# Performance work log

Hardware: AMD Instinct MI355X
Metric: run time of the kernel (lower is better)

## Reference

```python
import jax, jax.numpy as jnp
import numpy as np

B, C_ATT, C_VAL = 1, 64, 64
T, H, W = 40, 32, 32
HW = H * W
TOPK = 10
TEMP = 0.07
NEIGHBOR_RANGE = 24  # circle mode -> radius = 24 // 2
NON_MASK_LEN = 1     # first frame is not masked
NEG_INF = -1e30


def _spatial_neighbor_circle(h, w, neighbor_range):
    """Circle-mode spatial neighbor mask, (h*w, h*w) bool."""
    radius = neighbor_range // 2
    gy, gx = jnp.meshgrid(jnp.arange(h, dtype=jnp.float32),
                          jnp.arange(w, dtype=jnp.float32), indexing='ij')
    dy = gy[:, :, None, None] - gy[None, None, :, :]
    dx = gx[:, :, None, None] - gx[None, None, :, :]
    dist = jnp.sqrt(dy * dy + dx * dx)
    return (dist < radius).reshape(h * w, h * w)


def setup_inputs() -> dict:
    key0 = jax.random.key(0)
    k1, k2, k3 = jax.random.split(key0, 3)
    query = jax.random.normal(k1, (B, C_ATT, H, W), dtype=jnp.float32)
    key = jax.random.normal(k2, (B, C_ATT, T, H, W), dtype=jnp.float32)
    value = jax.random.normal(k3, (B, C_VAL, T, H, W), dtype=jnp.float32)
    mask = _spatial_neighbor_circle(H, W, NEIGHBOR_RANGE)  # (HW, HW) bool
    return {"query": query, "key": key, "value": value, "mask": mask}


def _l2_normalize(x, axis, eps=1e-12):
    # matches F.normalize(p=2): x / max(||x||, eps)
    n = jnp.sqrt(jnp.sum(x * x, axis=axis, keepdims=True))
    return x / jnp.maximum(n, eps)


def reference(query, key, value, mask):
    # normalize along channel dim
    q = _l2_normalize(query, axis=1).reshape(B, C_ATT, HW)          # (B,C,Q)
    k = _l2_normalize(key, axis=1).reshape(B, C_ATT, T * HW)        # (B,C,K)
    v = value.reshape(B, C_VAL, T * HW)                             # (B,Cv,K)

    # affinity over all keys vs all queries (chunking in the original is a
    # pure memory optimization; the math per query column is identical)
    aff = jnp.einsum('bck,bcq->bkq', k, q) / TEMP                   # (B,K,Q)

    # build full mask: first NON_MASK_LEN frames fully visible, remaining
    # frames restricted to the spatial-neighbor circle
    tiled = jnp.tile(mask, (T - NON_MASK_LEN, 1))                   # ((T-nm)*HW, Q)
    full_mask = jnp.concatenate(
        [jnp.ones((NON_MASK_LEN * HW, HW), dtype=bool), tiled], axis=0)  # (K,Q)
    aff = jnp.where(full_mask[None], aff, NEG_INF)

    # top-k over the key dimension, per query
    aff_qk = jnp.swapaxes(aff, 1, 2)                                # (B,Q,K)
    top_vals, top_idx = jax.lax.top_k(aff_qk, TOPK)                 # (B,Q,topk)
    weights = jax.nn.softmax(top_vals, axis=-1)                     # (B,Q,topk)

    # gather top-k values: (B,Cv,Q,topk)
    gathered = jnp.take_along_axis(v[:, :, None, :], top_idx[:, None, :, :], axis=3)
    out = jnp.einsum('bcqk,bqk->bcq', gathered, weights)            # (B,Cv,Q)
    return out.reshape(B, C_VAL, H, W)
```

## Files before the change

### kernel.cpp

```cpp
#include <hip/hip_runtime.h>
#include <hip/hip_bf16.h>
#include <float.h>

#define HWQ   1024
#define NK    40960
#define NCH   64
#define NTOP  10
#define NF0JOB 8
#define PVLEN (NF0JOB * NTOP)
#define CAPG  384
#define R2    144
#define TOTU  23556
#define NBLK  4096
#define TSCALE 14.2857142857142857f
#define LOSCL  4.8828125e-4f

typedef _Float16 f16x8 __attribute__((ext_vector_type(8)));
typedef float    f32x4 __attribute__((ext_vector_type(4)));
typedef unsigned short us8 __attribute__((ext_vector_type(8)));
typedef unsigned long long u64;
typedef unsigned int       u32;

__device__ inline float bf16bits_to_f32(unsigned short u) {
    union { u32 i; float f; } z; z.i = ((u32)u) << 16; return z.f;
}
__device__ inline unsigned short f32_to_bf16bits(float x) {
    __hip_bfloat16 b = __float2bfloat16(x);
    return *(unsigned short*)&b;
}

__device__ inline int sniff_fp32(const unsigned short* __restrict__ raw) {
    const int lane = threadIdx.x & 63;
    const int e = (raw[lane] >> 7) & 0xFF;
    const u64 m = __ballot(e < 100 || e > 133);
    return __popcll(m) > 16;
}

__device__ inline u32 ord32(float v) {
    const u32 b = __float_as_uint(v);
    return b ^ (u32)(((int)b >> 31) | (int)0x80000000);
}
__device__ inline u64 pack_vi(float val, int kidx) {
    return ((u64)ord32(val) << 16) | (u32)(0xFFFF - kidx);
}
__device__ inline float unpack_val(u64 p) {
    const u32 u = (u32)(p >> 16);
    const u32 b = u ^ (~((u32)((int)u >> 31)) | 0x80000000u);
    return __uint_as_float(b);
}
__device__ inline int unpack_idx(u64 p) { return 0xFFFF - (int)(p & 0xFFFF); }

__device__ inline void ins10(u64* v, u64 pk) {
#pragma unroll
    for (int j = NTOP - 1; j >= 1; --j) {
        const bool gj = pk > v[j];
        const bool gp = pk > v[j - 1];
        v[j] = gj ? (gp ? v[j - 1] : pk) : v[j];
    }
    if (pk > v[0]) v[0] = pk;
}

__global__ __launch_bounds__(256) void prep_all(
    const void* __restrict__ qin_, const void* __restrict__ kin_,
    const void* __restrict__ vin_,
    f16x8* __restrict__ kh, f16x8* __restrict__ kl,
    f16x8* __restrict__ qh, f16x8* __restrict__ ql,
    unsigned short* __restrict__ vt, int* __restrict__ cnt)
{
    __shared__ float ssq[4][64];
    const int isf  = sniff_fp32((const unsigned short*)kin_);
    const int bid  = blockIdx.x;
    const int tid  = threadIdx.x;
    const int w    = tid >> 6;
    const int lane = tid & 63;
    const int c0   = w * 16;

    if (bid == 655) {
        cnt[tid * 4 + 0] = 0; cnt[tid * 4 + 1] = 0;
        cnt[tid * 4 + 2] = 0; cnt[tid * 4 + 3] = 0;
    }

    if (bid < 640) {
        const int key = bid * 64 + lane;
        float x[16];
        if (isf) {
            const float* p = (const float*)kin_;
#pragma unroll
            for (int i = 0; i < 16; ++i) x[i] = p[(c0 + i) * NK + key];
        } else {
            const __hip_bfloat16* p = (const __hip_bfloat16*)kin_;
#pragma unroll
            for (int i = 0; i < 16; ++i) x[i] = __bfloat162float(p[(c0 + i) * NK + key]);
        }
        float s = 0.f;
#pragma unroll
        for (int i = 0; i < 16; ++i) s = fmaf(x[i], x[i], s);
        ssq[w][lane] = s;
        __syncthreads();
        s = ssq[0][lane] + ssq[1][lane] + ssq[2][lane] + ssq[3][lane];
        const float rn = 1.0f / fmaxf(sqrtf(s), 1e-12f);

        const int tb = (key >> 4) * 128 + (key & 15);
#pragma unroll
        for (int b2 = 0; b2 < 2; ++b2) {
            f16x8 h, l;
#pragma unroll
            for (int jj = 0; jj < 8; ++jj) {
                const float xv = x[b2 * 8 + jj] * rn;
                const _Float16 hh = (_Float16)xv;
                h[jj] = hh;
                l[jj] = (_Float16)((xv - (float)hh) * 2048.0f);
            }
            kh[tb + (w * 2 + b2) * 16] = h;
            kl[tb + (w * 2 + b2) * 16] = l;
        }

        unsigned short vv[16];
        if (isf) {
            const float* p = (const float*)vin_;
#pragma unroll
            for (int i = 0; i < 16; ++i) vv[i] = f32_to_bf16bits(p[(c0 + i) * NK + key]);
        } else {
            const unsigned short* p = (const unsigned short*)vin_;
#pragma unroll
            for (int i = 0; i < 16; ++i) vv[i] = p[(c0 + i) * NK + key];
        }
        us8* dst = (us8*)(vt + (size_t)key * NCH + c0);
#pragma unroll
        for (int b2 = 0; b2 < 2; ++b2) {
            us8 o;
#pragma unroll
            for (int e = 0; e < 8; ++e) o[e] = vv[b2 * 8 + e];
            dst[b2] = o;
        }
    } else {
        const int q = (bid - 640) * 64 + lane;
        float x[16];
        if (isf) {
            const float* p = (const float*)qin_;
#pragma unroll
            for (int i = 0; i < 16; ++i) x[i] = p[(c0 + i) * HWQ + q];
        } else {
            const __hip_bfloat16* p = (const __hip_bfloat16*)qin_;
#pragma unroll
            for (int i = 0; i < 16; ++i) x[i] = __bfloat162float(p[(c0 + i) * HWQ + q]);
        }
        float s = 0.f;
#pragma unroll
        for (int i = 0; i < 16; ++i) s = fmaf(x[i], x[i], s);
        ssq[w][lane] = s;
        __syncthreads();
        s = ssq[0][lane] + ssq[1][lane] + ssq[2][lane] + ssq[3][lane];
        const float rn = 1.0f / fmaxf(sqrtf(s), 1e-12f);

        const int tb = (q >> 4) * 128 + (q & 15);
#pragma unroll
        for (int b2 = 0; b2 < 2; ++b2) {
            f16x8 h, l;
#pragma unroll
            for (int jj = 0; jj < 8; ++jj) {
                const float xv = x[b2 * 8 + jj] * rn;
                const _Float16 hh = (_Float16)xv;
                h[jj] = hh;
                l[jj] = (_Float16)((xv - (float)hh) * 2048.0f);
            }
            qh[tb + (w * 2 + b2) * 16] = h;
            ql[tb + (w * 2 + b2) * 16] = l;
        }
    }
}

__device__ inline void quad_merge_store(
    u64 (*sm)[16][NTOP], int lane, u64* out10)
{
    int p0 = 0, p1 = 0, p2 = 0, p3 = 0;
#pragma unroll
    for (int r = 0; r < NTOP; ++r) {
        const u64 h0 = sm[0][lane][p0], h1 = sm[1][lane][p1];
        const u64 h2 = sm[2][lane][p2], h3 = sm[3][lane][p3];
        u64 m = h0; int sel = 0;
        if (h1 > m) { m = h1; sel = 1; }
        if (h2 > m) { m = h2; sel = 2; }
        if (h3 > m) { m = h3; sel = 3; }
        out10[r] = m;
        p0 += (sel == 0); p1 += (sel == 1); p2 += (sel == 2); p3 += (sel == 3);
    }
}

__global__ __launch_bounds__(128) void attn_f0(
    const f16x8* __restrict__ kh, const f16x8* __restrict__ kl,
    const f16x8* __restrict__ qh, const f16x8* __restrict__ ql,
    u64* __restrict__ pv)
{
    __shared__ u64 sm[2][4][16][NTOP];

    const int tid  = threadIdx.x;
    const int w    = tid >> 6;
    const int lane = tid & 63;
    const int quad = lane >> 4;
    const int n    = lane & 15;

    const int t   = blockIdx.x * 2 + w;
    const int job = blockIdx.y;

    const int qb = t * 128 + n;
    const f16x8 bh0 = qh[qb + quad * 16];
    const f16x8 bh1 = qh[qb + (4 + quad) * 16];
    const f16x8 bl0 = ql[qb + quad * 16];
    const f16x8 bl1 = ql[qb + (4 + quad) * 16];

    u64 v[NTOP];
#pragma unroll
    for (int jj = 0; jj < NTOP; ++jj) v[jj] = 0ull;

    const int start = job * 8, end = start + 8;
    const int loff = (n + quad * 16) * 16;
    const char* ph = (const char*)kh + (size_t)start * 2048 + loff;
    const char* pl = (const char*)kl + (size_t)start * 2048 + loff;

    for (int kt = start; kt < end; ++kt) {
        const f16x8 Ah0 = *(const f16x8*)(ph);
        const f16x8 Ah1 = *(const f16x8*)(ph + 1024);
        const f16x8 Al0 = *(const f16x8*)(pl);
        const f16x8 Al1 = *(const f16x8*)(pl + 1024);

        f32x4 accH = {0.f,0.f,0.f,0.f}, accL0 = {0.f,0.f,0.f,0.f}, accL1 = {0.f,0.f,0.f,0.f};
        accH  = __builtin_amdgcn_mfma_f32_16x16x32_f16(Ah0, bh0, accH, 0, 0, 0);
        accH  = __builtin_amdgcn_mfma_f32_16x16x32_f16(Ah1, bh1, accH, 0, 0, 0);
        accL0 = __builtin_amdgcn_mfma_f32_16x16x32_f16(Ah0, bl0, accL0, 0, 0, 0);
        accL0 = __builtin_amdgcn_mfma_f32_16x16x32_f16(Al0, bh0, accL0, 0, 0, 0);
        accL1 = __builtin_amdgcn_mfma_f32_16x16x32_f16(Ah1, bl1, accL1, 0, 0, 0);
        accL1 = __builtin_amdgcn_mfma_f32_16x16x32_f16(Al1, bh1, accL1, 0, 0, 0);

        const int key0 = kt * 16 + quad * 4;
#pragma unroll
        for (int r = 0; r < 4; ++r) {
            const float val = fmaf(accL0[r] + accL1[r], LOSCL, accH[r]);
            const u64 pk = pack_vi(val, key0 + r);
            if (pk > v[NTOP - 1]) ins10(v, pk);
        }
        ph += 2048; pl += 2048;
    }

#pragma unroll
    for (int jj = 0; jj < NTOP; ++jj) sm[w][quad][n][jj] = v[jj];
    __syncthreads();

    if (lane < 16) {
        u64 out10[NTOP];
        quad_merge_store(sm[w], lane, out10);
        const int q = t * 16 + lane;
#pragma unroll
        for (int r = 0; r < NTOP; ++r) pv[(size_t)q * PVLEN + job * NTOP + r] = out10[r];
    }
}

__global__ __launch_bounds__(256) void theta_refine(
    const u64* __restrict__ pv, float* __restrict__ thmax)
{
    const int q    = blockIdx.x * 4 + (threadIdx.x >> 6);
    const int lane = threadIdx.x & 63;

    u64 l0 = pv[(size_t)q * PVLEN + lane];
    u64 l1 = (lane < 16) ? pv[(size_t)q * PVLEN + 64 + lane] : 0ull;

    u64 m = 0ull;
#pragma unroll
    for (int r = 0; r < NTOP; ++r) {
        u64 c = l0 > l1 ? l0 : l1;
#pragma unroll
        for (int off = 32; off >= 1; off >>= 1) {
            const u32 lo = (u32)c, hi = (u32)(c >> 32);
            const u32 lo2 = (u32)__shfl_xor((int)lo, off);
            const u32 hi2 = (u32)__shfl_xor((int)hi, off);
            const u64 o = ((u64)hi2 << 32) | lo2;
            if (o > c) c = o;
        }
        if (l0 == c) l0 = 0ull;
        if (l1 == c) l1 = 0ull;
        m = c;
    }
    if (lane == 0) thmax[q] = unpack_val(m);
}

__global__ __launch_bounds__(64) void attn_masked(
    const f16x8* __restrict__ kh, const f16x8* __restrict__ kl,
    const f16x8* __restrict__ qh, const f16x8* __restrict__ ql,
    const float* __restrict__ thmax,
    u64* __restrict__ gcand, int* __restrict__ cnt)
{
    const int lane = threadIdx.x;
    const int quad = lane >> 4;
    const int n    = lane & 15;

    const int wid = (blockIdx.x & 7) * (NBLK / 8) + (blockIdx.x >> 3);
    const int u0  = (int)(((long long)wid * TOTU) >> 12);
    const int u1  = (int)(((long long)(wid + 1) * TOTU) >> 12);

    f16x8 b0h0, b0h1, b0l0, b0l1, b1h0, b1h1, b1l0, b1l1;
    float theta0 = 0.f, theta1 = 0.f;
    int cur_qy = -1, q0 = 0;

    for (int u = u0; u < u1; ++u) {
        const int fm1 = u / 604;
        const int rem = u - fm1 * 604;
        int qy, off;
        if (rem < 210) {
            int t = (int)((sqrtf((float)(529 + 8 * rem)) - 23.0f) * 0.5f);
            while ((t * (t + 23)) / 2 > rem) --t;
            while (((t + 1) * (t + 24)) / 2 <= rem) ++t;
            qy = t; off = rem - (t * (t + 23)) / 2;
        } else if (rem < 417) {
            qy = 12 + (rem - 210) / 23; off = (rem - 210) % 23;
        } else {
            const int s = 603 - rem;
            int t = (int)((sqrtf((float)(529 + 8 * s)) - 23.0f) * 0.5f);
            while ((t * (t + 23)) / 2 > s) --t;
            while (((t + 1) * (t + 24)) / 2 <= s) ++t;
            qy = 31 - t;
            off = (12 + t) - 1 - (s - (t * (t + 23)) / 2);
        }
        const int rlo = (qy > 11) ? qy - 11 : 0;
        const int row = rlo + off;
        const int frame = fm1 + 1;

        if (qy != cur_qy) {
            cur_qy = qy;
            const int qb = qy * 256 + n;
            b0h0 = qh[qb + quad * 16];       b0h1 = qh[qb + (4 + quad) * 16];
            b0l0 = ql[qb + quad * 16];       b0l1 = ql[qb + (4 + quad) * 16];
            b1h0 = qh[qb + 128 + quad * 16]; b1h1 = qh[qb + 128 + (4 + quad) * 16];
            b1l0 = ql[qb + 128 + quad * 16]; b1l1 = ql[qb + 128 + (4 + quad) * 16];
            q0 = qy * 32 + n;
            theta0 = thmax[q0];
            theta1 = thmax[q0 + 16];
        }

        const int dy   = row - qy;
        const int rem2 = R2 - dy * dy;
        const int tbase = frame * 64 + row * 2;
        const int keyrow = frame * 1024 + row * 32;

#pragma unroll 1
        for (int kt2 = 0; kt2 < 2; ++kt2) {
            const f16x8* pA = kh + (tbase + kt2) * 128 + n;
            const f16x8* pL = kl + (tbase + kt2) * 128 + n;
            const f16x8 ah0 = pA[quad * 16];
            const f16x8 ah1 = pA[(4 + quad) * 16];
            const f16x8 al0 = pL[quad * 16];
            const f16x8 al1 = pL[(4 + quad) * 16];

            f32x4 H0 = {0.f,0.f,0.f,0.f}, L00 = {0.f,0.f,0.f,0.f}, L01 = {0.f,0.f,0.f,0.f};
            f32x4 H1 = {0.f,0.f,0.f,0.f}, L10 = {0.f,0.f,0.f,0.f}, L11 = {0.f,0.f,0.f,0.f};
            H0  = __builtin_amdgcn_mfma_f32_16x16x32_f16(ah0, b0h0, H0, 0, 0, 0);
            H0  = __builtin_amdgcn_mfma_f32_16x16x32_f16(ah1, b0h1, H0, 0, 0, 0);
            L00 = __builtin_amdgcn_mfma_f32_16x16x32_f16(ah0, b0l0, L00, 0, 0, 0);
            L00 = __builtin_amdgcn_mfma_f32_16x16x32_f16(al0, b0h0, L00, 0, 0, 0);
            L01 = __builtin_amdgcn_mfma_f32_16x16x32_f16(ah1, b0l1, L01, 0, 0, 0);
            L01 = __builtin_amdgcn_mfma_f32_16x16x32_f16(al1, b0h1, L01, 0, 0, 0);
            H1  = __builtin_amdgcn_mfma_f32_16x16x32_f16(ah0, b1h0, H1, 0, 0, 0);
            H1  = __builtin_amdgcn_mfma_f32_16x16x32_f16(ah1, b1h1, H1, 0, 0, 0);
            L10 = __builtin_amdgcn_mfma_f32_16x16x32_f16(ah0, b1l0, L10, 0, 0, 0);
            L10 = __builtin_amdgcn_mfma_f32_16x16x32_f16(al0, b1h0, L10, 0, 0, 0);
            L11 = __builtin_amdgcn_mfma_f32_16x16x32_f16(ah1, b1l1, L11, 0, 0, 0);
            L11 = __builtin_amdgcn_mfma_f32_16x16x32_f16(al1, b1h1, L11, 0, 0, 0);

            const int kx0  = kt2 * 16 + quad * 4;
            const int key0 = keyrow + kx0;
#pragma unroll
            for (int r = 0; r < 4; ++r) {
                const float v0 = fmaf(L00[r] + L01[r], LOSCL, H0[r]);
                const float v1 = fmaf(L10[r] + L11[r], LOSCL, H1[r]);
                if (v0 > theta0) {
                    const int dx = kx0 + r - n;
                    if (dx * dx < rem2) {
                        const int pos = atomicAdd(&cnt[q0], 1);
                        if (pos < CAPG) gcand[(size_t)q0 * CAPG + pos] = pack_vi(v0, key0 + r);
                    }
                }
                if (v1 > theta1) {
                    const int dx = kx0 + r - 16 - n;
                    if (dx * dx < rem2) {
                        const int pos = atomicAdd(&cnt[q0 + 16], 1);
                        if (pos < CAPG) gcand[(size_t)(q0 + 16) * CAPG + pos] = pack_vi(v1, key0 + r);
                    }
                }
            }
        }
    }
}

__global__ __launch_bounds__(64) void finalize_kernel(
    const u64* __restrict__ pv, const u64* __restrict__ gcand,
    const int* __restrict__ cnt, const unsigned short* __restrict__ vt,
    const unsigned short* __restrict__ kin_raw, void* __restrict__ out_)
{
    const int isf  = sniff_fp32(kin_raw);
    const int q    = blockIdx.x;
    const int lane = threadIdx.x;

    u64 lv[8];
    lv[0] = pv[(size_t)q * PVLEN + lane];
    lv[1] = (lane < 16) ? pv[(size_t)q * PVLEN + 64 + lane] : 0ull;
    const int c = min(cnt[q], CAPG);
#pragma unroll
    for (int e = 0; e < 6; ++e) {
        const int idx = e * 64 + lane;
        lv[2 + e] = (idx < c) ? gcand[(size_t)q * CAPG + idx] : 0ull;
    }

    float wv[NTOP]; int wi[NTOP];
#pragma unroll
    for (int r = 0; r < NTOP; ++r) {
        u64 m = lv[0];
#pragma unroll
        for (int e = 1; e < 8; ++e) if (lv[e] > m) m = lv[e];
#pragma unroll
        for (int off = 32; off >= 1; off >>= 1) {
            const u32 lo = (u32)m, hi = (u32)(m >> 32);
            const u32 lo2 = (u32)__shfl_xor((int)lo, off);
            const u32 hi2 = (u32)__shfl_xor((int)hi, off);
            const u64 o = ((u64)hi2 << 32) | lo2;
            if (o > m) m = o;
        }
#pragma unroll
        for (int e = 0; e < 8; ++e) if (lv[e] == m) lv[e] = 0ull;
        wv[r] = unpack_val(m); wi[r] = unpack_idx(m);
    }

    float ww[NTOP]; float wsum = 0.f;
#pragma unroll
    for (int r = 0; r < NTOP; ++r) { ww[r] = expf((wv[r] - wv[0]) * TSCALE); wsum += ww[r]; }
    const float inv = 1.0f / wsum;

    float acc = 0.f;
#pragma unroll
    for (int r = 0; r < NTOP; ++r)
        acc += ww[r] * bf16bits_to_f32(vt[(size_t)wi[r] * NCH + lane]);
    const float res = acc * inv;

    if (isf) ((float*)out_)[lane * HWQ + q] = res;
    else     ((__hip_bfloat16*)out_)[lane * HWQ + q] = __float2bfloat16(res);
}

extern "C" void kernel_launch(void* const* d_in, const int* in_sizes, int n_in,
                              void* d_out, int out_size, void* d_ws, size_t ws_size,
                              hipStream_t stream)
{
    const void* qin = d_in[0];
    const void* kin = d_in[1];
    const void* vin = d_in[2];

    char* w = (char*)d_ws;
    f16x8*          kh    = (f16x8*)(w);
    f16x8*          kl    = (f16x8*)(w + 5242880);
    f16x8*          qhv   = (f16x8*)(w + 10485760);
    f16x8*          qlv   = (f16x8*)(w + 10616832);
    unsigned short* vt    = (unsigned short*)(w + 10747904);
    u64*            pv    = (u64*)(w + 15990784);
    u64*            gcand = (u64*)(w + 16646144);
    float*          thmax = (float*)(w + 19791872);
    int*            cnt   = (int*)(w + 19795968);

    prep_all<<<656, 256, 0, stream>>>(qin, kin, vin, kh, kl, qhv, qlv, vt, cnt);
    attn_f0<<<dim3(32, 8), 128, 0, stream>>>(kh, kl, qhv, qlv, pv);
    theta_refine<<<256, 256, 0, stream>>>(pv, thmax);
    attn_masked<<<NBLK, 64, 0, stream>>>(kh, kl, qhv, qlv, thmax, gcand, cnt);
    finalize_kernel<<<HWQ, 64, 0, stream>>>(pv, gcand, cnt, vt,
                                            (const unsigned short*)kin, d_out);
}
```

Measured before the change: 146.7 us.

## Fuse all stages into one cooperative persistent kernel with grid syncs

Replaces the five separate launches (prep, frame-0 attention, theta refine, masked attention, finalize) with a single cooperative kernel of 512 blocks. The stages are separated by grid-wide syncs. Frame-0 top-k is now done by 64 blocks with a four-wave merge, and the masked-candidate buffers are sharded per query (8 shards, padded counters) to reduce atomic contention. This is meant to remove launch gaps and inter-kernel overhead, at the cost of grid.sync latency, idle blocks during the frame-0 stage, and a smaller per-shard candidate capacity.

Measured after the change: 343.2 us. +134.0%, slower.

```diff
diff --git a/kernel.cpp b/kernel.cpp
--- a/kernel.cpp
+++ b/kernel.cpp
@@ -1,17 +1,18 @@
 #include <hip/hip_runtime.h>
+#include <hip/hip_cooperative_groups.h>
 #include <hip/hip_bf16.h>
 #include <float.h>
+
+namespace cg = cooperative_groups;
 
 #define HWQ   1024
 #define NK    40960
 #define NCH   64
 #define NTOP  10
-#define NF0JOB 8
-#define PVLEN (NF0JOB * NTOP)
-#define CAPG  384
+#define CAPS  64
 #define R2    144
 #define TOTU  23556
-#define NBLK  4096
+#define NWAVE 2048
 #define TSCALE 14.2857142857142857f
 #define LOSCL  4.8828125e-4f
 
@@ -60,124 +61,12 @@
     if (pk > v[0]) v[0] = pk;
 }
 
-__global__ __launch_bounds__(256) void prep_all(
-    const void* __restrict__ qin_, const void* __restrict__ kin_,
-    const void* __restrict__ vin_,
-    f16x8* __restrict__ kh, f16x8* __restrict__ kl,
-    f16x8* __restrict__ qh, f16x8* __restrict__ ql,
-    unsigned short* __restrict__ vt, int* __restrict__ cnt)
-{
-    __shared__ float ssq[4][64];
-    const int isf  = sniff_fp32((const unsigned short*)kin_);
-    const int bid  = blockIdx.x;
-    const int tid  = threadIdx.x;
-    const int w    = tid >> 6;
-    const int lane = tid & 63;
-    const int c0   = w * 16;
-
-    if (bid == 655) {
-        cnt[tid * 4 + 0] = 0; cnt[tid * 4 + 1] = 0;
-        cnt[tid * 4 + 2] = 0; cnt[tid * 4 + 3] = 0;
-    }
-
-    if (bid < 640) {
-        const int key = bid * 64 + lane;
-        float x[16];
-        if (isf) {
-            const float* p = (const float*)kin_;
-#pragma unroll
-            for (int i = 0; i < 16; ++i) x[i] = p[(c0 + i) * NK + key];
-        } else {
-            const __hip_bfloat16* p = (const __hip_bfloat16*)kin_;
-#pragma unroll
-            for (int i = 0; i < 16; ++i) x[i] = __bfloat162float(p[(c0 + i) * NK + key]);
-        }
-        float s = 0.f;
-#pragma unroll
-        for (int i = 0; i < 16; ++i) s = fmaf(x[i], x[i], s);
-        ssq[w][lane] = s;
-        __syncthreads();
-        s = ssq[0][lane] + ssq[1][lane] + ssq[2][lane] + ssq[3][lane];
-        const float rn = 1.0f / fmaxf(sqrtf(s), 1e-12f);
-
-        const int tb = (key >> 4) * 128 + (key & 15);
-#pragma unroll
-        for (int b2 = 0; b2 < 2; ++b2) {
-            f16x8 h, l;
-#pragma unroll
-            for (int jj = 0; jj < 8; ++jj) {
-                const float xv = x[b2 * 8 + jj] * rn;
-                const _Float16 hh = (_Float16)xv;
-                h[jj] = hh;
-                l[jj] = (_Float16)((xv - (float)hh) * 2048.0f);
-            }
-            kh[tb + (w * 2 + b2) * 16] = h;
-            kl[tb + (w * 2 + b2) * 16] = l;
-        }
-
-        unsigned short vv[16];
-        if (isf) {
-            const float* p = (const float*)vin_;
-#pragma unroll
-            for (int i = 0; i < 16; ++i) vv[i] = f32_to_bf16bits(p[(c0 + i) * NK + key]);
-        } else {
-            const unsigned short* p = (const unsigned short*)vin_;
-#pragma unroll
-            for (int i = 0; i < 16; ++i) vv[i] = p[(c0 + i) * NK + key];
-        }
-        us8* dst = (us8*)(vt + (size_t)key * NCH + c0);
-#pragma unroll
-        for (int b2 = 0; b2 < 2; ++b2) {
-            us8 o;
-#pragma unroll
-            for (int e = 0; e < 8; ++e) o[e] = vv[b2 * 8 + e];
-            dst[b2] = o;
-        }
-    } else {
-        const int q = (bid - 640) * 64 + lane;
-        float x[16];
-        if (isf) {
-            const float* p = (const float*)qin_;
-#pragma unroll
-            for (int i = 0; i < 16; ++i) x[i] = p[(c0 + i) * HWQ + q];
-        } else {
-            const __hip_bfloat16* p = (const __hip_bfloat16*)qin_;
-#pragma unroll
-            for (int i = 0; i < 16; ++i) x[i] = __bfloat162float(p[(c0 + i) * HWQ + q]);
-        }
-        float s = 0.f;
-#pragma unroll
-        for (int i = 0; i < 16; ++i) s = fmaf(x[i], x[i], s);
-        ssq[w][lane] = s;
-        __syncthreads();
-        s = ssq[0][lane] + ssq[1][lane] + ssq[2][lane] + ssq[3][lane];
-        const float rn = 1.0f / fmaxf(sqrtf(s), 1e-12f);
-
-        const int tb = (q >> 4) * 128 + (q & 15);
-#pragma unroll
-        for (int b2 = 0; b2 < 2; ++b2) {
-            f16x8 h, l;
-#pragma unroll
-            for (int jj = 0; jj < 8; ++jj) {
-                const float xv = x[b2 * 8 + jj] * rn;
-                const _Float16 hh = (_Float16)xv;
-                h[jj] = hh;
-                l[jj] = (_Float16)((xv - (float)hh) * 2048.0f);
-            }
-            qh[tb + (w * 2 + b2) * 16] = h;
-            ql[tb + (w * 2 + b2) * 16] = l;
-        }
-    }
-}
-
-__device__ inline void quad_merge_store(
-    u64 (*sm)[16][NTOP], int lane, u64* out10)
-{
+__device__ inline void merge4(const u64* base, int lane, u64* out10) {
     int p0 = 0, p1 = 0, p2 = 0, p3 = 0;
+    const u64* b = base + lane * 10;
 #pragma unroll
     for (int r = 0; r < NTOP; ++r) {
-        const u64 h0 = sm[0][lane][p0], h1 = sm[1][lane][p1];
-        const u64 h2 = sm[2][lane][p2], h3 = sm[3][lane][p3];
+        const u64 h0 = b[p0], h1 = b[160 + p1], h2 = b[320 + p2], h3 = b[480 + p3];
         u64 m = h0; int sel = 0;
         if (h1 > m) { m = h1; sel = 1; }
         if (h2 > m) { m = h2; sel = 2; }
@@ -187,260 +76,353 @@
     }
 }
 
-__global__ __launch_bounds__(128) void attn_f0(
-    const f16x8* __restrict__ kh, const f16x8* __restrict__ kl,
-    const f16x8* __restrict__ qh, const f16x8* __restrict__ ql,
-    u64* __restrict__ pv)
+__device__ inline void flush_cand(int* cnt, u64* gcand, int q, int shard, u64 pk) {
+    const int pos = atomicAdd(&cnt[q * 32 + shard], 1);
+    if (pos < CAPS) gcand[((size_t)q * 8 + shard) * CAPS + pos] = pk;
+}
+
+__global__ __launch_bounds__(256, 2) void fused_kernel(
+    const void* __restrict__ qin_, const void* __restrict__ kin_,
+    const void* __restrict__ vin_,
+    f16x8* __restrict__ kh, f16x8* __restrict__ kl,
+    f16x8* __restrict__ qh, f16x8* __restrict__ ql,
+    unsigned short* __restrict__ vt,
+    u64* __restrict__ pv, float* __restrict__ thmax,
+    u64* __restrict__ gcand, int* __restrict__ cnt,
+    void* __restrict__ out_)
 {
-    __shared__ u64 sm[2][4][16][NTOP];
-
+    __shared__ __align__(16) char shraw[25600];
+    cg::grid_group grid = cg::this_grid();
+
+    const int bid  = blockIdx.x;
     const int tid  = threadIdx.x;
     const int w    = tid >> 6;
     const int lane = tid & 63;
     const int quad = lane >> 4;
     const int n    = lane & 15;
-
-    const int t   = blockIdx.x * 2 + w;
-    const int job = blockIdx.y;
-
-    const int qb = t * 128 + n;
-    const f16x8 bh0 = qh[qb + quad * 16];
-    const f16x8 bh1 = qh[qb + (4 + quad) * 16];
-    const f16x8 bl0 = ql[qb + quad * 16];
-    const f16x8 bl1 = ql[qb + (4 + quad) * 16];
-
-    u64 v[NTOP];
-#pragma unroll
-    for (int jj = 0; jj < NTOP; ++jj) v[jj] = 0ull;
-
-    const int start = job * 8, end = start + 8;
-    const int loff = (n + quad * 16) * 16;
-    const char* ph = (const char*)kh + (size_t)start * 2048 + loff;
-    const char* pl = (const char*)kl + (size_t)start * 2048 + loff;
-
-    for (int kt = start; kt < end; ++kt) {
-        const f16x8 Ah0 = *(const f16x8*)(ph);
-        const f16x8 Ah1 = *(const f16x8*)(ph + 1024);
-        const f16x8 Al0 = *(const f16x8*)(pl);
-        const f16x8 Al1 = *(const f16x8*)(pl + 1024);
-
-        f32x4 accH = {0.f,0.f,0.f,0.f}, accL0 = {0.f,0.f,0.f,0.f}, accL1 = {0.f,0.f,0.f,0.f};
-        accH  = __builtin_amdgcn_mfma_f32_16x16x32_f16(Ah0, bh0, accH, 0, 0, 0);
-        accH  = __builtin_amdgcn_mfma_f32_16x16x32_f16(Ah1, bh1, accH, 0, 0, 0);
-        accL0 = __builtin_amdgcn_mfma_f32_16x16x32_f16(Ah0, bl0, accL0, 0, 0, 0);
-        accL0 = __builtin_amdgcn_mfma_f32_16x16x32_f16(Al0, bh0, accL0, 0, 0, 0);
-        accL1 = __builtin_amdgcn_mfma_f32_16x16x32_f16(Ah1, bl1, accL1, 0, 0, 0);
-        accL1 = __builtin_amdgcn_mfma_f32_16x16x32_f16(Al1, bh1, accL1, 0, 0, 0);
-
-        const int key0 = kt * 16 + quad * 4;
-#pragma unroll
-        for (int r = 0; r < 4; ++r) {
-            const float val = fmaf(accL0[r] + accL1[r], LOSCL, accH[r]);
-            const u64 pk = pack_vi(val, key0 + r);
-            if (pk > v[NTOP - 1]) ins10(v, pk);
+    const int isf  = sniff_fp32((const unsigned short*)kin_);
+
+    {
+        const int zi = bid * 256 + tid;
+        if (zi < 32768) cnt[zi] = 0;
+
+        float (*ssq)[64] = (float(*)[64])shraw;
+        const int c0 = w * 16;
+        for (int u = bid; u < 656; u += 512) {
+            if (u < 640) {
+                const int key = u * 64 + lane;
+                float x[16];
+                if (isf) {
+                    const float* p = (const float*)kin_;
+#pragma unroll
+                    for (int i = 0; i < 16; ++i) x[i] = p[(c0 + i) * NK + key];
+                } else {
+                    const __hip_bfloat16* p = (const __hip_bfloat16*)kin_;
+#pragma unroll
+                    for (int i = 0; i < 16; ++i) x[i] = __bfloat162float(p[(c0 + i) * NK + key]);
+                }
+                float s = 0.f;
+#pragma unroll
+                for (int i = 0; i < 16; ++i) s = fmaf(x[i], x[i], s);
+                ssq[w][lane] = s;
+                __syncthreads();
+                s = ssq[0][lane] + ssq[1][lane] + ssq[2][lane] + ssq[3][lane];
+                const float rn = 1.0f / fmaxf(sqrtf(s), 1e-12f);
+
+                const int tb = (key >> 4) * 128 + (key & 15);
+#pragma unroll
+                for (int b2 = 0; b2 < 2; ++b2) {
+                    f16x8 h, l;
+#pragma unroll
+                    for (int jj = 0; jj < 8; ++jj) {
+                        const float xv = x[b2 * 8 + jj] * rn;
+                        const _Float16 hh = (_Float16)xv;
+                        h[jj] = hh;
+                        l[jj] = (_Float16)((xv - (float)hh) * 2048.0f);
+                    }
+                    kh[tb + (w * 2 + b2) * 16] = h;
+                    kl[tb + (w * 2 + b2) * 16] = l;
+                }
+
+                unsigned short vv[16];
+                if (isf) {
+                    const float* p = (const float*)vin_;
+#pragma unroll
+                    for (int i = 0; i < 16; ++i) vv[i] = f32_to_bf16bits(p[(c0 + i) * NK + key]);
+                } else {
+                    const unsigned short* p = (const unsigned short*)vin_;
+#pragma unroll
+                    for (int i = 0; i < 16; ++i) vv[i] = p[(c0 + i) * NK + key];
+                }
+                us8* dst = (us8*)(vt + (size_t)key * NCH + c0);
+#pragma unroll
+                for (int b2 = 0; b2 < 2; ++b2) {
+                    us8 o;
+#pragma unroll
+                    for (int e = 0; e < 8; ++e) o[e] = vv[b2 * 8 + e];
+                    dst[b2] = o;
+                }
+                __syncthreads();
+            } else {
+                const int q = (u - 640) * 64 + lane;
+                float x[16];
+                if (isf) {
+                    const float* p = (const float*)qin_;
+#pragma unroll
+                    for (int i = 0; i < 16; ++i) x[i] = p[(c0 + i) * HWQ + q];
+                } else {
+                    const __hip_bfloat16* p = (const __hip_bfloat16*)qin_;
+#pragma unroll
+                    for (int i = 0; i < 16; ++i) x[i] = __bfloat162float(p[(c0 + i) * HWQ + q]);
+                }
+                float s = 0.f;
+#pragma unroll
+                for (int i = 0; i < 16; ++i) s = fmaf(x[i], x[i], s);
+                ssq[w][lane] = s;
+                __syncthreads();
+                s = ssq[0][lane] + ssq[1][lane] + ssq[2][lane] + ssq[3][lane];
+                const float rn = 1.0f / fmaxf(sqrtf(s), 1e-12f);
+
+                const int tb = (q >> 4) * 128 + (q & 15);
+#pragma unroll
+                for (int b2 = 0; b2 < 2; ++b2) {
+                    f16x8 h, l;
+#pragma unroll
+                    for (int jj = 0; jj < 8; ++jj) {
+                        const float xv = x[b2 * 8 + jj] * rn;
+                        const _Float16 hh = (_Float16)xv;
+                        h[jj] = hh;
+                        l[jj] = (_Float16)((xv - (float)hh) * 2048.0f);
+                    }
+                    qh[tb + (w * 2 + b2) * 16] = h;
+                    ql[tb + (w * 2 + b2) * 16] = l;
+                }
+                __syncthreads();
+            }
         }
-        ph += 2048; pl += 2048;
-    }
-
-#pragma unroll
-    for (int jj = 0; jj < NTOP; ++jj) sm[w][quad][n][jj] = v[jj];
-    __syncthreads();
-
-    if (lane < 16) {
-        u64 out10[NTOP];
-        quad_merge_store(sm[w], lane, out10);
-        const int q = t * 16 + lane;
-#pragma unroll
-        for (int r = 0; r < NTOP; ++r) pv[(size_t)q * PVLEN + job * NTOP + r] = out10[r];
-    }
-}
-
-__global__ __launch_bounds__(256) void theta_refine(
-    const u64* __restrict__ pv, float* __restrict__ thmax)
-{
-    const int q    = blockIdx.x * 4 + (threadIdx.x >> 6);
-    const int lane = threadIdx.x & 63;
-
-    u64 l0 = pv[(size_t)q * PVLEN + lane];
-    u64 l1 = (lane < 16) ? pv[(size_t)q * PVLEN + 64 + lane] : 0ull;
-
-    u64 m = 0ull;
-#pragma unroll
-    for (int r = 0; r < NTOP; ++r) {
-        u64 c = l0 > l1 ? l0 : l1;
-#pragma unroll
-        for (int off = 32; off >= 1; off >>= 1) {
-            const u32 lo = (u32)c, hi = (u32)(c >> 32);
-            const u32 lo2 = (u32)__shfl_xor((int)lo, off);
-            const u32 hi2 = (u32)__shfl_xor((int)hi, off);
-            const u64 o = ((u64)hi2 << 32) | lo2;
-            if (o > c) c = o;
+    }
+
+    grid.sync();
+
+    {
+        u64* smb = (u64*)shraw;
+        u64* wmb = (u64*)(shraw + 20480);
+
+        if (bid < 64) {
+            const int t = bid;
+            const int qb = t * 128 + n;
+            const f16x8 bh0 = qh[qb + quad * 16];
+            const f16x8 bh1 = qh[qb + (4 + quad) * 16];
+            const f16x8 bl0 = ql[qb + quad * 16];
+            const f16x8 bl1 = ql[qb + (4 + quad) * 16];
+
+            u64 v[NTOP];
+#pragma unroll
+            for (int jj = 0; jj < NTOP; ++jj) v[jj] = 0ull;
+
+            const int start = w * 16, end = start + 16;
+            const int loff = (n + quad * 16) * 16;
+            const char* ph = (const char*)kh + (size_t)start * 2048 + loff;
+            const char* pl = (const char*)kl + (size_t)start * 2048 + loff;
+
+            for (int kt = start; kt < end; ++kt) {
+                const f16x8 Ah0 = *(const f16x8*)(ph);
+                const f16x8 Ah1 = *(const f16x8*)(ph + 1024);
+                const f16x8 Al0 = *(const f16x8*)(pl);
+                const f16x8 Al1 = *(const f16x8*)(pl + 1024);
+
+                f32x4 aH = {0.f,0.f,0.f,0.f}, aL0 = {0.f,0.f,0.f,0.f}, aL1 = {0.f,0.f,0.f,0.f};
+                aH  = __builtin_amdgcn_mfma_f32_16x16x32_f16(Ah0, bh0, aH, 0, 0, 0);
+                aH  = __builtin_amdgcn_mfma_f32_16x16x32_f16(Ah1, bh1, aH, 0, 0, 0);
+                aL0 = __builtin_amdgcn_mfma_f32_16x16x32_f16(Ah0, bl0, aL0, 0, 0, 0);
+                aL0 = __builtin_amdgcn_mfma_f32_16x16x32_f16(Al0, bh0, aL0, 0, 0, 0);
+                aL1 = __builtin_amdgcn_mfma_f32_16x16x32_f16(Ah1, bl1, aL1, 0, 0, 0);
+                aL1 = __builtin_amdgcn_mfma_f32_16x16x32_f16(Al1, bh1, aL1, 0, 0, 0);
+
+                const int key0 = kt * 16 + quad * 4;
+#pragma unroll
+                for (int r = 0; r < 4; ++r) {
+                    const float val = fmaf(aL0[r] + aL1[r], LOSCL, aH[r]);
+                    const u64 pk = pack_vi(val, key0 + r);
+                    if (pk > v[NTOP - 1]) ins10(v, pk);
+                }
+                ph += 2048; pl += 2048;
+            }
+
+#pragma unroll
+            for (int jj = 0; jj < NTOP; ++jj)
+                smb[(size_t)w * 640 + (quad * 16 + n) * 10 + jj] = v[jj];
+            if (lane < 16) {
+                u64 o10[NTOP];
+                merge4(smb + (size_t)w * 640, lane, o10);
+#pragma unroll
+                for (int r = 0; r < NTOP; ++r) wmb[(size_t)w * 160 + lane * 10 + r] = o10[r];
+            }
         }
-        if (l0 == c) l0 = 0ull;
-        if (l1 == c) l1 = 0ull;
-        m = c;
-    }
-    if (lane == 0) thmax[q] = unpack_val(m);
-}
-
-__global__ __launch_bounds__(64) void attn_masked(
-    const f16x8* __restrict__ kh, const f16x8* __restrict__ kl,
-    const f16x8* __restrict__ qh, const f16x8* __restrict__ ql,
-    const float* __restrict__ thmax,
-    u64* __restrict__ gcand, int* __restrict__ cnt)
-{
-    const int lane = threadIdx.x;
-    const int quad = lane >> 4;
-    const int n    = lane & 15;
-
-    const int wid = (blockIdx.x & 7) * (NBLK / 8) + (blockIdx.x >> 3);
-    const int u0  = (int)(((long long)wid * TOTU) >> 12);
-    const int u1  = (int)(((long long)(wid + 1) * TOTU) >> 12);
-
-    f16x8 b0h0, b0h1, b0l0, b0l1, b1h0, b1h1, b1l0, b1l1;
-    float theta0 = 0.f, theta1 = 0.f;
-    int cur_qy = -1, q0 = 0;
-
-    for (int u = u0; u < u1; ++u) {
-        const int fm1 = u / 604;
-        const int rem = u - fm1 * 604;
-        int qy, off;
-        if (rem < 210) {
-            int t = (int)((sqrtf((float)(529 + 8 * rem)) - 23.0f) * 0.5f);
-            while ((t * (t + 23)) / 2 > rem) --t;
-            while (((t + 1) * (t + 24)) / 2 <= rem) ++t;
-            qy = t; off = rem - (t * (t + 23)) / 2;
-        } else if (rem < 417) {
-            qy = 12 + (rem - 210) / 23; off = (rem - 210) % 23;
-        } else {
-            const int s = 603 - rem;
-            int t = (int)((sqrtf((float)(529 + 8 * s)) - 23.0f) * 0.5f);
-            while ((t * (t + 23)) / 2 > s) --t;
-            while (((t + 1) * (t + 24)) / 2 <= s) ++t;
-            qy = 31 - t;
-            off = (12 + t) - 1 - (s - (t * (t + 23)) / 2);
+        __syncthreads();
+        if (bid < 64 && tid < 16) {
+            u64 o10[NTOP];
+            merge4(wmb, tid, o10);
+            const int q = bid * 16 + tid;
+#pragma unroll
+            for (int r = 0; r < NTOP; ++r) pv[(size_t)q * NTOP + r] = o10[r];
+            thmax[q] = unpack_val(o10[9]);
         }
-        const int rlo = (qy > 11) ? qy - 11 : 0;
-        const int row = rlo + off;
-        const int frame = fm1 + 1;
-
-        if (qy != cur_qy) {
-            cur_qy = qy;
-            const int qb = qy * 256 + n;
-            b0h0 = qh[qb + quad * 16];       b0h1 = qh[qb + (4 + quad) * 16];
-            b0l0 = ql[qb + quad * 16];       b0l1 = ql[qb + (4 + quad) * 16];
-            b1h0 = qh[qb + 128 + quad * 16]; b1h1 = qh[qb + 128 + (4 + quad) * 16];
-            b1l0 = ql[qb + 128 + quad * 16]; b1l1 = ql[qb + 128 + (4 + quad) * 16];
-            q0 = qy * 32 + n;
-            theta0 = thmax[q0];
-            theta1 = thmax[q0 + 16];
+    }
+
+    grid.sync();
+
+    {
+        const int wid = ((bid & 7) * 64 + (bid >> 3)) * 4 + w;
+        const int u0  = (int)(((long long)wid * TOTU) >> 11);
+        const int u1  = (int)(((long long)(wid + 1) * TOTU) >> 11);
+
+        f16x8 b0h0, b0h1, b0l0, b0l1, b1h0, b1h1, b1l0, b1l1;
+        float theta0 = 0.f, theta1 = 0.f;
+        int cur_qy = -1, q0 = 0;
+
+        for (int u = u0; u < u1; ++u) {
+            const int fm1 = u / 604;
+            const int rem = u - fm1 * 604;
+            int qy, off;
+            if (rem < 210) {
+                int t = (int)((sqrtf((float)(529 + 8 * rem)) - 23.0f) * 0.5f);
+                while ((t * (t + 23)) / 2 > rem) --t;
+                while (((t + 1) * (t + 24)) / 2 <= rem) ++t;
+                qy = t; off = rem - (t * (t + 23)) / 2;
+            } else if (rem < 417) {
+                qy = 12 + (rem - 210) / 23; off = (rem - 210) % 23;
+            } else {
+                const int s = 603 - rem;
+                int t = (int)((sqrtf((float)(529 + 8 * s)) - 23.0f) * 0.5f);
+                while ((t * (t + 23)) / 2 > s) --t;
+                while (((t + 1) * (t + 24)) / 2 <= s) ++t;
+                qy = 31 - t;
+                off = (12 + t) - 1 - (s - (t * (t + 23)) / 2);
+            }
+            const int rlo = (qy > 11) ? qy - 11 : 0;
+            const int row = rlo + off;
+            const int frame = fm1 + 1;
+            const int shard = fm1 / 5;
+
+            if (qy != cur_qy) {
+                cur_qy = qy;
+                const int qb = qy * 256 + n;
+                b0h0 = qh[qb + quad * 16];       b0h1 = qh[qb + (4 + quad) * 16];
+                b0l0 = ql[qb + quad * 16];       b0l1 = ql[qb + (4 + quad) * 16];
+                b1h0 = qh[qb + 128 + quad * 16]; b1h1 = qh[qb + 128 + (4 + quad) * 16];
+                b1l0 = ql[qb + 128 + quad * 16]; b1l1 = ql[qb + 128 + (4 + quad) * 16];
+                q0 = qy * 32 + n;
+                theta0 = thmax[q0];
+                theta1 = thmax[q0 + 16];
+            }
+
+            const int dy    = row - qy;
+            const int rem2  = R2 - dy * dy;
+            const int tbase = frame * 64 + row * 2;
+            const int keyrow = frame * 1024 + row * 32;
+
+            u64 s0 = 0ull, s1 = 0ull;
+
+#pragma unroll 1
+            for (int kt2 = 0; kt2 < 2; ++kt2) {
+                const f16x8* pA = kh + (tbase + kt2) * 128 + n;
+                const f16x8* pL = kl + (tbase + kt2) * 128 + n;
+                const f16x8 ah0 = pA[quad * 16];
+                const f16x8 ah1 = pA[(4 + quad) * 16];
+                const f16x8 al0 = pL[quad * 16];
+                const f16x8 al1 = pL[(4 + quad) * 16];
+
+                f32x4 H0 = {0.f,0.f,0.f,0.f}, L00 = {0.f,0.f,0.f,0.f}, L01 = {0.f,0.f,0.f,0.f};
+                f32x4 H1 = {0.f,0.f,0.f,0.f}, L10 = {0.f,0.f,0.f,0.f}, L11 = {0.f,0.f,0.f,0.f};
+                H0  = __builtin_amdgcn_mfma_f32_16x16x32_f16(ah0, b0h0, H0, 0, 0, 0);
+                H0  = __builtin_amdgcn_mfma_f32_16x16x32_f16(ah1, b0h1, H0, 0, 0, 0);
+                L00 = __builtin_amdgcn_mfma_f32_16x16x32_f16(ah0, b0l0, L00, 0, 0, 0);
+                L00 = __builtin_amdgcn_mfma_f32_16x16x32_f16(al0, b0h0, L00, 0, 0, 0);
+                L01 = __builtin_amdgcn_mfma_f32_16x16x32_f16(ah1, b0l1, L01, 0, 0, 0);
+                L01 = __builtin_amdgcn_mfma_f32_16x16x32_f16(al1, b0h1, L01, 0, 0, 0);
+                H1  = __builtin_amdgcn_mfma_f32_16x16x32_f16(ah0, b1h0, H1, 0, 0, 0);
+                H1  = __builtin_amdgcn_mfma_f32_16x16x32_f16(ah1, b1h1, H1, 0, 0, 0);
+                L10 = __builtin_amdgcn_mfma_f32_16x16x32_f16(ah0, b1l0, L10, 0, 0, 0);
+                L10 = __builtin_amdgcn_mfma_f32_16x16x32_f16(al0, b1h0, L10, 0, 0, 0);
+                L11 = __builtin_amdgcn_mfma_f32_16x16x32_f16(ah1, b1l1, L11, 0, 0, 0);
+                L11 = __builtin_amdgcn_mfma_f32_16x16x32_f16(al1, b1h1, L11, 0, 0, 0);
+
+                const int kx0  = kt2 * 16 + quad * 4;
+                const int key0 = keyrow + kx0;
+#pragma unroll
+                for (int r = 0; r < 4; ++r) {
+                    const float v0 = fmaf(L00[r] + L01[r], LOSCL, H0[r]);
+                    const float v1 = fmaf(L10[r] + L11[r], LOSCL, H1[r]);
+                    if (v0 > theta0) {
+                        const int dx = kx0 + r - n;
+                        if (dx * dx < rem2) {
+                            if (s0) flush_cand(cnt, gcand, q0, shard, s0);
+                            s0 = pack_vi(v0, key0 + r);
+                        }
+                    }
+                    if (v1 > theta1) {
+                        const int dx = kx0 + r - 16 - n;
+                        if (dx * dx < rem2) {
+                            if (s1) flush_cand(cnt, gcand, q0 + 16, shard, s1);
+                            s1 = pack_vi(v1, key0 + r);
+                        }
+                    }
+                }
+            }
+            if (s0) flush_cand(cnt, gcand, q0, shard, s0);
+            if (s1) flush_cand(cnt, gcand, q0 + 16, shard, s1);
         }
-
-        const int dy   = row - qy;
-        const int rem2 = R2 - dy * dy;
-        const int tbase = frame * 64 + row * 2;
-        const int keyrow = frame * 1024 + row * 32;
-
-#pragma unroll 1
-        for (int kt2 = 0; kt2 < 2; ++kt2) {
-            const f16x8* pA = kh + (tbase + kt2) * 128 + n;
-            const f16x8* pL = kl + (tbase + kt2) * 128 + n;
-            const f16x8 ah0 = pA[quad * 16];
-            const f16x8 ah1 = pA[(4 + quad) * 16];
-            const f16x8 al0 = pL[quad * 16];
-            const f16x8 al1 = pL[(4 + quad) * 16];
-
-            f32x4 H0 = {0.f,0.f,0.f,0.f}, L00 = {0.f,0.f,0.f,0.f}, L01 = {0.f,0.f,0.f,0.f};
-            f32x4 H1 = {0.f,0.f,0.f,0.f}, L10 = {0.f,0.f,0.f,0.f}, L11 = {0.f,0.f,0.f,0.f};
-            H0  = __builtin_amdgcn_mfma_f32_16x16x32_f16(ah0, b0h0, H0, 0, 0, 0);
-            H0  = __builtin_amdgcn_mfma_f32_16x16x32_f16(ah1, b0h1, H0, 0, 0, 0);
-            L00 = __builtin_amdgcn_mfma_f32_16x16x32_f16(ah0, b0l0, L00, 0, 0, 0);
-            L00 = __builtin_amdgcn_mfma_f32_16x16x32_f16(al0, b0h0, L00, 0, 0, 0);
-            L01 = __builtin_amdgcn_mfma_f32_16x16x32_f16(ah1, b0l1, L01, 0, 0, 0);
-            L01 = __builtin_amdgcn_mfma_f32_16x16x32_f16(al1, b0h1, L01, 0, 0, 0);
-            H1  = __builtin_amdgcn_mfma_f32_16x16x32_f16(ah0, b1h0, H1, 0, 0, 0);
-            H1  = __builtin_amdgcn_mfma_f32_16x16x32_f16(ah1, b1h1, H1, 0, 0, 0);
-            L10 = __builtin_amdgcn_mfma_f32_16x16x32_f16(ah0, b1l0, L10, 0, 0, 0);
-            L10 = __builtin_amdgcn_mfma_f32_16x16x32_f16(al0, b1h0, L10, 0, 0, 0);
-            L11 = __builtin_amdgcn_mfma_f32_16x16x32_f16(ah1, b1l1, L11, 0, 0, 0);
-            L11 = __builtin_amdgcn_mfma_f32_16x16x32_f16(al1, b1h1, L11, 0, 0, 0);
-
-            const int kx0  = kt2 * 16 + quad * 4;
-            const int key0 = keyrow + kx0;
-#pragma unroll
-            for (int r = 0; r < 4; ++r) {
-                const float v0 = fmaf(L00[r] + L01[r], LOSCL, H0[r]);
-                const float v1 = fmaf(L10[r] + L11[r], LOSCL, H1[r]);
-                if (v0 > theta0) {
-                    const int dx = kx0 + r - n;
-                    if (dx * dx < rem2) {
-                        const int pos = atomicAdd(&cnt[q0], 1);
-                        if (pos < CAPG) gcand[(size_t)q0 * CAPG + pos] = pack_vi(v0, key0 + r);
-                    }
-                }
-                if (v1 > theta1) {
-                    const int dx = kx0 + r - 16 - n;
-                    if (dx * dx < rem2) {
-                        const int pos = atomicAdd(&cnt[q0 + 16], 1);
-                        if (pos < CAPG) gcand[(size_t)(q0 + 16) * CAPG + pos] = pack_vi(v1, key0 + r);
-                    }
-                }
-            }
+    }
+
+    grid.sync();
+
+    {
+        const int q = bid * 4 + w;
+        if (q < HWQ) {
+            u64 lv[9];
+            lv[0] = (lane < NTOP) ? pv[(size_t)q * NTOP + lane] : 0ull;
+#pragma unroll
+            for (int e = 0; e < 8; ++e) {
+                const int c = cnt[q * 32 + e];
+                const int cc = c < CAPS ? c : CAPS;
+                lv[1 + e] = (lane < cc) ? gcand[((size_t)q * 8 + e) * CAPS + lane] : 0ull;
+            }
+
+            float wv[NTOP]; int wi[NTOP];
+#pragma unroll
+            for (int r = 0; r < NTOP; ++r) {
+                u64 m = lv[0];
+#pragma unroll
+                for (int e = 1; e < 9; ++e) if (lv[e] > m) m = lv[e];
+#pragma unroll
+                for (int off = 32; off >= 1; off >>= 1) {
+                    const u32 lo = (u32)m, hi = (u32)(m >> 32);
+                    const u32 lo2 = (u32)__shfl_xor((int)lo, off);
+                    const u32 hi2 = (u32)__shfl_xor((int)hi, off);
+                    const u64 o = ((u64)hi2 << 32) | lo2;
+                    if (o > m) m = o;
+                }
+#pragma unroll
+                for (int e = 0; e < 9; ++e) if (lv[e] == m) lv[e] = 0ull;
+                wv[r] = unpack_val(m); wi[r] = unpack_idx(m);
+            }
+
+            float ww[NTOP]; float wsum = 0.f;
+#pragma unroll
+            for (int r = 0; r < NTOP; ++r) { ww[r] = expf((wv[r] - wv[0]) * TSCALE); wsum += ww[r]; }
+            const float inv = 1.0f / wsum;
+
+            float acc = 0.f;
+#pragma unroll
+            for (int r = 0; r < NTOP; ++r)
+                acc += ww[r] * bf16bits_to_f32(vt[(size_t)wi[r] * NCH + lane]);
+            const float res = acc * inv;
+
+            if (isf) ((float*)out_)[lane * HWQ + q] = res;
+            else     ((__hip_bfloat16*)out_)[lane * HWQ + q] = __float2bfloat16(res);
         }
     }
-}
-
-__global__ __launch_bounds__(64) void finalize_kernel(
-    const u64* __restrict__ pv, const u64* __restrict__ gcand,
-    const int* __restrict__ cnt, const unsigned short* __restrict__ vt,
-    const unsigned short* __restrict__ kin_raw, void* __restrict__ out_)
-{
-    const int isf  = sniff_fp32(kin_raw);
-    const int q    = blockIdx.x;
-    const int lane = threadIdx.x;
-
-    u64 lv[8];
-    lv[0] = pv[(size_t)q * PVLEN + lane];
-    lv[1] = (lane < 16) ? pv[(size_t)q * PVLEN + 64 + lane] : 0ull;
-    const int c = min(cnt[q], CAPG);
-#pragma unroll
-    for (int e = 0; e < 6; ++e) {
-        const int idx = e * 64 + lane;
-        lv[2 + e] = (idx < c) ? gcand[(size_t)q * CAPG + idx] : 0ull;
-    }
-
-    float wv[NTOP]; int wi[NTOP];
-#pragma unroll
-    for (int r = 0; r < NTOP; ++r) {
-        u64 m = lv[0];
-#pragma unroll
-        for (int e = 1; e < 8; ++e) if (lv[e] > m) m = lv[e];
-#pragma unroll
-        for (int off = 32; off >= 1; off >>= 1) {
-            const u32 lo = (u32)m, hi = (u32)(m >> 32);
-            const u32 lo2 = (u32)__shfl_xor((int)lo, off);
-            const u32 hi2 = (u32)__shfl_xor((int)hi, off);
-            const u64 o = ((u64)hi2 << 32) | lo2;
-            if (o > m) m = o;
-        }
-#pragma unroll
-        for (int e = 0; e < 8; ++e) if (lv[e] == m) lv[e] = 0ull;
-        wv[r] = unpack_val(m); wi[r] = unpack_idx(m);
-    }
-
-    float ww[NTOP]; float wsum = 0.f;
-#pragma unroll
-    for (int r = 0; r < NTOP; ++r) { ww[r] = expf((wv[r] - wv[0]) * TSCALE); wsum += ww[r]; }
-    const float inv = 1.0f / wsum;
-
-    float acc = 0.f;
-#pragma unroll
-    for (int r = 0; r < NTOP; ++r)
-        acc += ww[r] * bf16bits_to_f32(vt[(size_t)wi[r] * NCH + lane]);
-    const float res = acc * inv;
-
-    if (isf) ((float*)out_)[lane * HWQ + q] = res;
-    else     ((__hip_bfloat16*)out_)[lane * HWQ + q] = __float2bfloat16(res);
 }
 
 extern "C" void kernel_launch(void* const* d_in, const int* in_sizes, int n_in,
@@ -451,21 +433,24 @@
     const void* kin = d_in[1];
     const void* vin = d_in[2];
 
-    char* w = (char*)d_ws;
-    f16x8*          kh    = (f16x8*)(w);
-    f16x8*          kl    = (f16x8*)(w + 5242880);
-    f16x8*          qhv   = (f16x8*)(w + 10485760);
-    f16x8*          qlv   = (f16x8*)(w + 10616832);
-    unsigned short* vt    = (unsigned short*)(w + 10747904);
-    u64*            pv    = (u64*)(w + 15990784);
-    u64*            gcand = (u64*)(w + 16646144);
-    float*          thmax = (float*)(w + 19791872);
-    int*            cnt   = (int*)(w + 19795968);
-
-    prep_all<<<656, 256, 0, stream>>>(qin, kin, vin, kh, kl, qhv, qlv, vt, cnt);
-    attn_f0<<<dim3(32, 8), 128, 0, stream>>>(kh, kl, qhv, qlv, pv);
-    theta_refine<<<256, 256, 0, stream>>>(pv, thmax);
-    attn_masked<<<NBLK, 64, 0, stream>>>(kh, kl, qhv, qlv, thmax, gcand, cnt);
-    finalize_kernel<<<HWQ, 64, 0, stream>>>(pv, gcand, cnt, vt,
-                                            (const unsigned short*)kin, d_out);
-}
+    char* wsp = (char*)d_ws;
+    f16x8*          kh    = (f16x8*)(wsp);
+    f16x8*          kl    = (f16x8*)(wsp + 5242880);
+    f16x8*          qhv   = (f16x8*)(wsp + 10485760);
+    f16x8*          qlv   = (f16x8*)(wsp + 10616832);
+    unsigned short* vt    = (unsigned short*)(wsp + 10747904);
+    u64*            pv    = (u64*)(wsp + 15990784);
+    float*          thmax = (float*)(wsp + 16072704);
+    u64*            gcand = (u64*)(wsp + 16076800);
+    int*            cnt   = (int*)(wsp + 20271104);
+
+    void* out = d_out;
+    void* args[] = {
+        (void*)&qin, (void*)&kin, (void*)&vin,
+        (void*)&kh, (void*)&kl, (void*)&qhv, (void*)&qlv,
+        (void*)&vt, (void*)&pv, (void*)&thmax,
+        (void*)&gcand, (void*)&cnt, (void*)&out
+    };
+    hipLaunchCooperativeKernel((const void*)fused_kernel,
+                               dim3(512), dim3(256), args, 0, stream);
+}
```

## Buffer masked-attention candidates per wave in LDS before global atomic flush

Applied to the files above, without the earlier changes.

Candidate (value, index) pairs that pass the threshold are first appended to a per-wave, per-query shared-memory buffer using LDS atomics. When the query row changes, and again at the end, they are flushed to global memory with one global atomicAdd per query. This replaces many contended global atomics with cheap local ones. The kernel now runs four waves per 256-thread block with a quarter of the blocks, and the inner key-tile loop is unrolled. The local buffer holds at most 16 candidates per query per segment and silently drops any extra, which is a correctness risk if more candidates pass the threshold.

Result: faster. 121.0 us (-17.5%).

```diff
diff --git a/kernel.cpp b/kernel.cpp
--- a/kernel.cpp
+++ b/kernel.cpp
@@ -9,9 +9,10 @@
 #define NF0JOB 8
 #define PVLEN (NF0JOB * NTOP)
 #define CAPG  384
+#define CAPW  16
 #define R2    144
 #define TOTU  23556
-#define NBLK  4096
+#define NBLK  1024
 #define TSCALE 14.2857142857142857f
 #define LOSCL  4.8828125e-4f
 
@@ -283,19 +284,27 @@
     if (lane == 0) thmax[q] = unpack_val(m);
 }
 
-__global__ __launch_bounds__(64) void attn_masked(
+__global__ __launch_bounds__(256, 4) void attn_masked(
     const f16x8* __restrict__ kh, const f16x8* __restrict__ kl,
     const f16x8* __restrict__ qh, const f16x8* __restrict__ ql,
     const float* __restrict__ thmax,
     u64* __restrict__ gcand, int* __restrict__ cnt)
 {
-    const int lane = threadIdx.x;
+    __shared__ u64 wcand[4][32][CAPW];
+    __shared__ int wcnt[4][32];
+
+    const int tid  = threadIdx.x;
+    const int w    = tid >> 6;
+    const int lane = tid & 63;
     const int quad = lane >> 4;
     const int n    = lane & 15;
 
-    const int wid = (blockIdx.x & 7) * (NBLK / 8) + (blockIdx.x >> 3);
-    const int u0  = (int)(((long long)wid * TOTU) >> 12);
-    const int u1  = (int)(((long long)(wid + 1) * TOTU) >> 12);
+    if (lane < 32) wcnt[w][lane] = 0;
+
+    const int bidx = ((int)blockIdx.x & 7) * (NBLK / 8) + ((int)blockIdx.x >> 3);
+    const int wid  = bidx * 4 + w;
+    const int u0   = (int)(((long long)wid * TOTU) >> 12);
+    const int u1   = (int)(((long long)(wid + 1) * TOTU) >> 12);
 
     f16x8 b0h0, b0h1, b0l0, b0l1, b1h0, b1h1, b1l0, b1l1;
     float theta0 = 0.f, theta1 = 0.f;
@@ -325,6 +334,22 @@
         const int frame = fm1 + 1;
 
         if (qy != cur_qy) {
+            if (cur_qy >= 0) {
+                __builtin_amdgcn_wave_barrier();
+                if (lane < 32) {
+                    const int rc = min(wcnt[w][lane], CAPW);
+                    if (rc > 0) {
+                        const int qq = cur_qy * 32 + lane;
+                        const int base = atomicAdd(&cnt[qq], rc);
+                        for (int jf = 0; jf < rc; ++jf) {
+                            const int pos = base + jf;
+                            if (pos < CAPG) gcand[(size_t)qq * CAPG + pos] = wcand[w][lane][jf];
+                        }
+                    }
+                    wcnt[w][lane] = 0;
+                }
+                __builtin_amdgcn_wave_barrier();
+            }
             cur_qy = qy;
             const int qb = qy * 256 + n;
             b0h0 = qh[qb + quad * 16];       b0h1 = qh[qb + (4 + quad) * 16];
@@ -336,12 +361,12 @@
             theta1 = thmax[q0 + 16];
         }
 
-        const int dy   = row - qy;
-        const int rem2 = R2 - dy * dy;
+        const int dy    = row - qy;
+        const int rem2  = R2 - dy * dy;
         const int tbase = frame * 64 + row * 2;
         const int keyrow = frame * 1024 + row * 32;
 
-#pragma unroll 1
+#pragma unroll
         for (int kt2 = 0; kt2 < 2; ++kt2) {
             const f16x8* pA = kh + (tbase + kt2) * 128 + n;
             const f16x8* pL = kl + (tbase + kt2) * 128 + n;
@@ -374,17 +399,30 @@
                 if (v0 > theta0) {
                     const int dx = kx0 + r - n;
                     if (dx * dx < rem2) {
-                        const int pos = atomicAdd(&cnt[q0], 1);
-                        if (pos < CAPG) gcand[(size_t)q0 * CAPG + pos] = pack_vi(v0, key0 + r);
+                        const int pos = atomicAdd(&wcnt[w][n], 1);
+                        if (pos < CAPW) wcand[w][n][pos] = pack_vi(v0, key0 + r);
                     }
                 }
                 if (v1 > theta1) {
                     const int dx = kx0 + r - 16 - n;
                     if (dx * dx < rem2) {
-                        const int pos = atomicAdd(&cnt[q0 + 16], 1);
-                        if (pos < CAPG) gcand[(size_t)(q0 + 16) * CAPG + pos] = pack_vi(v1, key0 + r);
+                        const int pos = atomicAdd(&wcnt[w][16 + n], 1);
+                        if (pos < CAPW) wcand[w][16 + n][pos] = pack_vi(v1, key0 + r);
                     }
                 }
+            }
+        }
+    }
+
+    __builtin_amdgcn_wave_barrier();
+    if (cur_qy >= 0 && lane < 32) {
+        const int rc = min(wcnt[w][lane], CAPW);
+        if (rc > 0) {
+            const int qq = cur_qy * 32 + lane;
+            const int base = atomicAdd(&cnt[qq], rc);
+            for (int jf = 0; jf < rc; ++jf) {
+                const int pos = base + jf;
+                if (pos < CAPG) gcand[(size_t)qq * CAPG + pos] = wcand[w][lane][jf];
             }
         }
     }
@@ -465,7 +503,7 @@
     prep_all<<<656, 256, 0, stream>>>(qin, kin, vin, kh, kl, qhv, qlv, vt, cnt);
     attn_f0<<<dim3(32, 8), 128, 0, stream>>>(kh, kl, qhv, qlv, pv);
     theta_refine<<<256, 256, 0, stream>>>(pv, thmax);
-    attn_masked<<<NBLK, 64, 0, stream>>>(kh, kl, qhv, qlv, thmax, gcand, cnt);
+    attn_masked<<<NBLK, 256, 0, stream>>>(kh, kl, qhv, qlv, thmax, gcand, cnt);
     finalize_kernel<<<HWQ, 64, 0, stream>>>(pv, gcand, cnt, vt,
                                             (const unsigned short*)kin, d_out);
 }
```
